# Kernel tuning notes

Hardware: AMD Instinct MI355X
Metric: run time of the kernel (lower is better)

The kernel has to match this reference:

```python
import jax, jax.numpy as jnp
import numpy as np

B, S, F, D, H, L, FF, M, NH, D2, O = 4, 1024, 20, 512, 8, 4, 2048, 32, 3, 256, 1
HD = D // H


def ln(x, g, b, eps=1e-5):
    m = jnp.mean(x, -1, keepdims=True)
    v = jnp.mean((x - m) ** 2, -1, keepdims=True)
    return (x - m) / jnp.sqrt(v + eps) * g + b


def posenc(seq_len, d_model):
    pos = jnp.arange(seq_len, dtype=jnp.float32)[:, None]
    div = jnp.exp(jnp.arange(0, d_model, 2, dtype=jnp.float32) * (-np.log(10000.0) / d_model))
    pe = jnp.zeros((seq_len, d_model), jnp.float32)
    pe = pe.at[:, 0::2].set(jnp.sin(pos * div)).at[:, 1::2].set(jnp.cos(pos * div))
    return pe


def setup_inputs():
    key = jax.random.key(0)
    ks = iter(jax.random.split(key, 64))
    g = lambda shape, s=0.02: jax.random.normal(next(ks), shape, jnp.float32) * s
    z = lambda shape: jnp.zeros(shape, jnp.float32)
    o = lambda shape: jnp.ones(shape, jnp.float32)
    return {
        'x': jax.random.normal(next(ks), (B, S, F), jnp.float32),
        'in_W': g((F, D)), 'in_b': z((D,)), 'in_ln_g': o((D,)), 'in_ln_b': z((D,)),
        'ln1_g': o((L, D)), 'ln1_b': z((L, D)),
        'Wq': g((L, D, D)), 'bq': z((L, D)), 'Wk': g((L, D, D)), 'bk': z((L, D)),
        'Wv': g((L, D, D)), 'bv': z((L, D)), 'Wo': g((L, D, D)), 'bo': z((L, D)),
        'rel': g((L, 2 * M + 1, HD)),
        'ln2_g': o((L, D)), 'ln2_b': z((L, D)),
        'W1': g((L, D, FF)), 'b1': z((L, FF)), 'W2': g((L, FF, D)), 'b2': z((L, D)),
        'gWq': g((D, D)), 'gbq': z((D,)), 'gWk': g((D, D)), 'gbk': z((D,)),
        'gWv': g((D, D)), 'gbv': z((D,)), 'gWo': g((D, D)), 'gbo': z((D,)),
        'hW1': g((NH, D, D2)), 'hb1': z((NH, D2)), 'hln_g': o((NH, D2)), 'hln_b': z((NH, D2)),
        'hW2': g((NH, D2, O)), 'hb2': z((NH, O)),
    }


def _heads(xx, Wq, bq, Wk, bk, Wv, bv):
    # project and split into heads -> [B,H,S,HD]
    q = (xx @ Wq + bq).reshape(B, S, H, HD).transpose(0, 2, 1, 3)
    k = (xx @ Wk + bk).reshape(B, S, H, HD).transpose(0, 2, 1, 3)
    v = (xx @ Wv + bv).reshape(B, S, H, HD).transpose(0, 2, 1, 3)
    return q, k, v


def _block(x, l1g, l1b, Wq, bq, Wk, bk, Wv, bv, Wo, bo, rel, l2g, l2b, W1, b1, W2, b2):
    xn = ln(x, l1g, l1b)
    q, k, v = _heads(xn, Wq, bq, Wk, bk, Wv, bv)
    scores = jnp.einsum('bhqd,bhkd->bhqk', q, k) / jnp.sqrt(jnp.float32(HD))
    pos = jnp.arange(S)
    rel_idx = jnp.clip(pos[None, :] - pos[:, None], -M, M) + M  # [S,S]
    rel_enc = rel[rel_idx]  # [S,S,HD]
    # relative-position bias (NOT scaled by sqrt(HD), matching the torch code)
    scores = scores + jnp.einsum('bhqd,qkd->bhqk', q, rel_enc)
    w = jax.nn.softmax(scores, axis=-1)
    out = jnp.einsum('bhqk,bhkd->bhqd', w, v).transpose(0, 2, 1, 3).reshape(B, S, D)
    x = x + out @ Wo + bo
    xn = ln(x, l2g, l2b)
    ff = jax.nn.gelu(xn @ W1 + b1, approximate=False) @ W2 + b2
    return x + ff


def _forward(x, in_W, in_b, in_ln_g, in_ln_b, ln1_g, ln1_b, Wq, bq, Wk, bk, Wv, bv, Wo, bo, rel,
             ln2_g, ln2_b, W1, b1, W2, b2, gWq, gbq, gWk, gbk, gWv, gbv, gWo, gbo,
             hW1, hb1, hln_g, hln_b, hW2, hb2):
    h = ln(x @ in_W + in_b, in_ln_g, in_ln_b)
    h = h + posenc(S, D)[None]
    for l in range(L):
        h = _block(h, ln1_g[l], ln1_b[l], Wq[l], bq[l], Wk[l], bk[l], Wv[l], bv[l],
                   Wo[l], bo[l], rel[l], ln2_g[l], ln2_b[l], W1[l], b1[l], W2[l], b2[l])
    # global multi-head self-attention (standard scaled dot-product)
    q, k, v = _heads(h, gWq, gbq, gWk, gbk, gWv, gbv)
    w = jax.nn.softmax(jnp.einsum('bhqd,bhkd->bhqk', q, k) / jnp.sqrt(jnp.float32(HD)), axis=-1)
    go = jnp.einsum('bhqk,bhkd->bhqd', w, v).transpose(0, 2, 1, 3).reshape(B, S, D) @ gWo + gbo
    ctx = go[:, -1, :]  # last-timestep context [B,D]
    y = jnp.einsum('bd,hde->bhe', ctx, hW1) + hb1  # [B,NH,D2]
    y = jax.nn.relu(ln(y, hln_g, hln_b))
    return jnp.einsum('bhe,heo->bho', y, hW2) + hb2  # [B,NH,O]


def reference(x, in_W, in_b, in_ln_g, in_ln_b, ln1_g, ln1_b, Wq, bq, Wk, bk, Wv, bv, Wo, bo, rel,
              ln2_g, ln2_b, W1, b1, W2, b2, gWq, gbq, gWk, gbk, gWv, gbv, gWo, gbo,
              hW1, hb1, hln_g, hln_b, hW2, hb2):
    return _forward(x, in_W, in_b, in_ln_g, in_ln_b, ln1_g, ln1_b, Wq, bq, Wk, bk, Wv, bv, Wo, bo,
                    rel, ln2_g, ln2_b, W1, b1, W2, b2, gWq, gbq, gWk, gbk, gWv, gbv, gWo, gbo,
                    hW1, hb1, hln_g, hln_b, hW2, hb2)
```

## Files before the change

kernel.cpp:

```cpp
#include <hip/hip_runtime.h>
#include <math.h>

#define DEV __device__ __forceinline__

constexpr int BSD = 4 * 1024 * 512;

typedef __attribute__((ext_vector_type(8))) short bf16x8;
typedef __attribute__((ext_vector_type(4))) float f32x4;

typedef __attribute__((address_space(1))) const void global_cvoid;
typedef __attribute__((address_space(3))) void lds_void;

DEV ushort f2b(float f) {
  union { float f; uint u; } x{f};
  uint r = x.u + 0x7fff + ((x.u >> 16) & 1);
  return (ushort)(r >> 16);
}
DEV float b2f(ushort u) {
  union { uint u; float f; } x{(uint)u << 16};
  return x.f;
}
DEV int swz128(int b) { return b ^ (((b >> 7) & 7) << 4); }

DEV float wave_sum(float v) {
#pragma unroll
  for (int m = 32; m >= 1; m >>= 1) v += __shfl_xor(v, m, 64);
  return v;
}
DEV float wave_max(float v) {
#pragma unroll
  for (int m = 32; m >= 1; m >>= 1) v = fmaxf(v, __shfl_xor(v, m, 64));
  return v;
}
DEV float block_sum(float v, float* sm) {
  v = wave_sum(v);
  __syncthreads();
  if ((threadIdx.x & 63) == 0) sm[threadIdx.x >> 6] = v;
  __syncthreads();
  return sm[0] + sm[1] + sm[2] + sm[3];
}
DEV float block_max(float v, float* sm) {
  v = wave_max(v);
  __syncthreads();
  if ((threadIdx.x & 63) == 0) sm[threadIdx.x >> 6] = v;
  __syncthreads();
  return fmaxf(fmaxf(sm[0], sm[1]), fmaxf(sm[2], sm[3]));
}

__global__ __launch_bounds__(256) void k_inproj(
    const float* __restrict__ x, const float* __restrict__ W,
    const float* __restrict__ bias, const float* __restrict__ g,
    const float* __restrict__ bt, float* __restrict__ h) {
  int r = blockIdx.x;
  int s = r & 1023;
  int t = threadIdx.x;
  __shared__ float xr[20];
  __shared__ float red[4];
  if (t < 20) xr[t] = x[r * 20 + t];
  __syncthreads();
  float o0 = bias[t], o1 = bias[t + 256];
#pragma unroll
  for (int f = 0; f < 20; f++) {
    float xv = xr[f];
    o0 += xv * W[f * 512 + t];
    o1 += xv * W[f * 512 + t + 256];
  }
  float mean = block_sum(o0 + o1, red) * (1.f / 512.f);
  float d0 = o0 - mean, d1 = o1 - mean;
  float var = block_sum(d0 * d0 + d1 * d1, red) * (1.f / 512.f);
  float rs = rsqrtf(var + 1e-5f);
  float n0 = d0 * rs * g[t] + bt[t];
  float n1 = d1 * rs * g[t + 256] + bt[t + 256];
  const float c1 = -9.210340371976184f / 512.f;
  {
    int c = t;
    float div = expf((float)(c & ~1) * c1);
    float arg = (float)s * div;
    n0 += (c & 1) ? cosf(arg) : sinf(arg);
  }
  {
    int c = t + 256;
    float div = expf((float)(c & ~1) * c1);
    float arg = (float)s * div;
    n1 += (c & 1) ? cosf(arg) : sinf(arg);
  }
  float* hr = h + (size_t)r * 512;
  hr[t] = n0;
  hr[t + 256] = n1;
}

__global__ __launch_bounds__(256) void k_lnw(
    const float* __restrict__ x, const float* __restrict__ g,
    const float* __restrict__ bt, ushort* __restrict__ y) {
  int lane = threadIdx.x & 63;
  int r = blockIdx.x * 4 + (threadIdx.x >> 6);
  const float4* xr = (const float4*)(x + (size_t)r * 512);
  float4 a = xr[lane];
  float4 c = xr[lane + 64];
  float s = a.x + a.y + a.z + a.w + c.x + c.y + c.z + c.w;
  float mean = wave_sum(s) * (1.f / 512.f);
  float d0 = a.x - mean, d1 = a.y - mean, d2 = a.z - mean, d3 = a.w - mean;
  float e0 = c.x - mean, e1 = c.y - mean, e2 = c.z - mean, e3 = c.w - mean;
  float vs = d0 * d0 + d1 * d1 + d2 * d2 + d3 * d3 +
             e0 * e0 + e1 * e1 + e2 * e2 + e3 * e3;
  float var = wave_sum(vs) * (1.f / 512.f);
  float rs = rsqrtf(var + 1e-5f);
  const float4* g4 = (const float4*)g;
  const float4* b4 = (const float4*)bt;
  float4 g0 = g4[lane], g1 = g4[lane + 64];
  float4 b0 = b4[lane], b1 = b4[lane + 64];
  ushort4 o0 = {f2b(d0 * rs * g0.x + b0.x), f2b(d1 * rs * g0.y + b0.y),
                f2b(d2 * rs * g0.z + b0.z), f2b(d3 * rs * g0.w + b0.w)};
  ushort4 o1 = {f2b(e0 * rs * g1.x + b1.x), f2b(e1 * rs * g1.y + b1.y),
                f2b(e2 * rs * g1.z + b1.z), f2b(e3 * rs * g1.w + b1.w)};
  ushort4* yr = (ushort4*)(y + (size_t)r * 512);
  yr[lane] = o0;
  yr[lane + 64] = o1;
}

struct PJobs {
  const float* s[19];
  ushort* d[19];
};
__global__ __launch_bounds__(256) void k_wprep(PJobs j, int K, int N) {
  const float* src = j.s[blockIdx.z];
  ushort* dst = j.d[blockIdx.z];
  __shared__ float ld[32][33];
  int n0 = blockIdx.x * 32, k0 = blockIdx.y * 32;
  int c = threadIdx.x & 31, r0 = threadIdx.x >> 5;
#pragma unroll
  for (int i = 0; i < 4; i++)
    ld[r0 + i * 8][c] = src[(size_t)(k0 + r0 + i * 8) * N + n0 + c];
  __syncthreads();
#pragma unroll
  for (int i = 0; i < 4; i++)
    dst[(size_t)(n0 + r0 + i * 8) * K + k0 + c] = f2b(ld[c][r0 + i * 8]);
}

__global__ __launch_bounds__(256) void k_relprep(const float* __restrict__ rel,
                                                 ushort* __restrict__ relb) {
  int i = blockIdx.x * 256 + threadIdx.x;
  int l = blockIdx.y;
  int r = i >> 6, d = i & 63;
  float v = (r < 65) ? rel[((size_t)l * 65 + r) * 64 + d] * 8.f : 0.f;
  relb[(size_t)l * 80 * 64 + i] = f2b(v);
}

template <int BM, int BN, int MODE, int FUSEB>
__global__ __launch_bounds__(256) void k_mg(
    const ushort* __restrict__ A, const ushort* __restrict__ Bt,
    const float* __restrict__ bias0, const float* __restrict__ bias1,
    const float* __restrict__ bias2, void* __restrict__ Cv,
    ushort* __restrict__ C2, int K, int ldc, int gx) {
  __shared__ __align__(16) ushort As[2][BM * 64];
  __shared__ __align__(16) ushort Bs[2][BN * 64];
  int nwg = gridDim.x;
  int id = blockIdx.x;
  int logical = (id & 7) * (nwg >> 3) + (id >> 3);
  int bx = logical % gx, by = logical / gx;
  int row0 = by * BM, col0 = bx * BN;
  int t = threadIdx.x, lane = t & 63, w = t >> 6;
  int rl15 = lane & 15, l16 = lane >> 4;
  constexpr int WR = (BM == 128 && BN == 128) ? 2 : BM / 32;
  constexpr int WC = 4 / WR;
  constexpr int MI = BM / (WR * 16);
  constexpr int NI = BN / (WC * 16);
  int wr = w % WR, wc = w / WR;
  int wrow = wr * MI * 16;
  int wcol = wc * NI * 16;
  f32x4 acc[MI][NI] = {};

  auto stage = [&](int buf, int kb) {
#pragma unroll
    for (int i = 0; i < BM / 32; i++) {
      int blk = w * (BM / 32) + i;
      int lb = blk * 1024 + lane * 16;
      int lg = swz128(lb);
      int r = lg >> 7, cb = (lg & 127) >> 1;
      __builtin_amdgcn_global_load_lds(
          (global_cvoid*)(A + (size_t)(row0 + r) * K + kb + cb),
          (lds_void*)((char*)As[buf] + blk * 1024), 16, 0, 0);
    }
#pragma unroll
    for (int i = 0; i < BN / 32; i++) {
      int blk = w * (BN / 32) + i;
      int lb = blk * 1024 + lane * 16;
      int lg = swz128(lb);
      int r = lg >> 7, cb = (lg & 127) >> 1;
      __builtin_amdgcn_global_load_lds(
          (global_cvoid*)(Bt + (size_t)(col0 + r) * K + kb + cb),
          (lds_void*)((char*)Bs[buf] + blk * 1024), 16, 0, 0);
    }
  };

  stage(0, 0);
  __syncthreads();
  int nkt = K >> 6;
  for (int kt = 0; kt < nkt; kt++) {
    int cur = kt & 1;
    if (kt + 1 < nkt) stage(cur ^ 1, (kt + 1) << 6);
#pragma unroll
    for (int ks = 0; ks < 2; ks++) {
      bf16x8 af[MI], bfr[NI];
#pragma unroll
      for (int mi = 0; mi < MI; mi++) {
        int row = wrow + mi * 16 + rl15;
        af[mi] =
            *(const bf16x8*)((char*)As[cur] + swz128(row * 128 + ks * 64 + l16 * 16));
      }
#pragma unroll
      for (int ni = 0; ni < NI; ni++) {
        int row = wcol + ni * 16 + rl15;
        bfr[ni] =
            *(const bf16x8*)((char*)Bs[cur] + swz128(row * 128 + ks * 64 + l16 * 16));
      }
#pragma unroll
      for (int mi = 0; mi < MI; mi++)
#pragma unroll
        for (int ni = 0; ni < NI; ni++)
          acc[mi][ni] = __builtin_amdgcn_mfma_f32_16x16x32_bf16(af[mi], bfr[ni],
                                                                acc[mi][ni], 0, 0, 0);
    }
    __syncthreads();
  }
#pragma unroll
  for (int mi = 0; mi < MI; mi++) {
#pragma unroll
    for (int ni = 0; ni < NI; ni++) {
      int col = col0 + wcol + ni * 16 + rl15;
      float bv;
      if (FUSEB) {
        const float* bp = bias0;
        int c = col;
        if (c >= 1024) { bp = bias2; c -= 1024; }
        else if (c >= 512) { bp = bias1; c -= 512; }
        bv = bp[c];
      } else {
        bv = bias0[col];
      }
#pragma unroll
      for (int r = 0; r < 4; r++) {
        int row = row0 + wrow + mi * 16 + l16 * 4 + r;
        float val = acc[mi][ni][r] + bv;
        if (FUSEB && col < 512) val *= 0.125f;
        if (MODE == 0) {
          ushort bval = f2b(val);
          ((ushort*)Cv)[(size_t)row * ldc + col] = bval;
          if (FUSEB && col >= 1024) {
            int dg = col - 1024;
            int bh = (row >> 10) * 8 + (dg >> 6);
            C2[((size_t)bh * 64 + (dg & 63)) * 1024 + (row & 1023)] = bval;
          }
        } else if (MODE == 1) {
          float* Cp = (float*)Cv + (size_t)row * ldc + col;
          *Cp = *Cp + val;
        } else if (MODE == 2) {
          val = 0.5f * val * (1.f + erff(val * 0.70710678118654752f));
          ((ushort*)Cv)[(size_t)row * ldc + col] = f2b(val);
        } else {
          float* Cp = (float*)Cv + (size_t)row * ldc + col;
          float nv = *Cp + val;
          *Cp = nv;
          C2[(size_t)row * ldc + col] = f2b(nv);
        }
      }
    }
  }
}

__global__ __launch_bounds__(256) void k_attn3(
    const ushort* __restrict__ qkv, const ushort* __restrict__ vT,
    const ushort* __restrict__ relb, ushort* __restrict__ ao) {
  __shared__ __align__(16) ushort Ks[2][64 * 64];
  __shared__ __align__(16) ushort Vts[2][64 * 64];
  __shared__ ushort qrlb[4][16][66];
  __shared__ __align__(16) ushort Pl[4][16 * 72];
  int t = threadIdx.x, lane = t & 63, w = t >> 6;
  int bid = blockIdx.x;
  int p = bid & 31;
  int h = p & 7, b = p >> 3;
  int q0 = (bid >> 5) * 64;
  int qw = q0 + w * 16;
  int rl15 = lane & 15, l16 = lane >> 4;
  size_t baseq = ((size_t)b * 1024) * 1536 + h * 64;
  size_t basek = baseq + 512;
  const ushort* vTb = vT + ((size_t)(b * 8 + h)) * 64 * 1024;

  bf16x8 aq[2];
#pragma unroll
  for (int ks = 0; ks < 2; ks++)
    aq[ks] = *(const bf16x8*)(qkv + baseq + (size_t)(qw + rl15) * 1536 + ks * 32 + l16 * 8);

#pragma unroll
  for (int nb = 0; nb < 5; nb++) {
    f32x4 rc = {};
#pragma unroll
    for (int ks = 0; ks < 2; ks++) {
      bf16x8 rb =
          *(const bf16x8*)(relb + (size_t)(nb * 16 + rl15) * 64 + ks * 32 + l16 * 8);
      rc = __builtin_amdgcn_mfma_f32_16x16x32_bf16(aq[ks], rb, rc, 0, 0, 0);
    }
    int col = nb * 16 + rl15;
    if (col < 65) {
#pragma unroll
      for (int r = 0; r < 4; r++) qrlb[w][l16 * 4 + r][col] = f2b(rc[r]);
    }
  }

  auto stage = [&](int buf, int kb) {
#pragma unroll
    for (int i = 0; i < 2; i++) {
      int blk = w * 2 + i;
      int lb = blk * 1024 + lane * 16;
      int lg = swz128(lb);
      int r = lg >> 7, cb = (lg & 127) >> 1;
      __builtin_amdgcn_global_load_lds(
          (global_cvoid*)(qkv + basek + (size_t)(kb + r) * 1536 + cb),
          (lds_void*)((char*)Ks[buf] + blk * 1024), 16, 0, 0);
      __builtin_amdgcn_global_load_lds(
          (global_cvoid*)(vTb + (size_t)r * 1024 + kb + cb),
          (lds_void*)((char*)Vts[buf] + blk * 1024), 16, 0, 0);
    }
  };

  float m_own = -1e30f, l_own = 0.f;
  f32x4 oacc[4] = {};

  stage(0, 0);
  __syncthreads();

  for (int kt = 0; kt < 16; kt++) {
    int kb = kt << 6;
    int cur = kt & 1;
    if (kt < 15) stage(cur ^ 1, kb + 64);

    f32x4 sacc[4] = {};
#pragma unroll
    for (int ks = 0; ks < 2; ks++) {
#pragma unroll
      for (int nb = 0; nb < 4; nb++) {
        bf16x8 kf = *(const bf16x8*)((char*)Ks[cur] +
                                     swz128((nb * 16 + rl15) * 128 + ks * 64 + l16 * 16));
        sacc[nb] = __builtin_amdgcn_mfma_f32_16x16x32_bf16(kf, aq[ks], sacc[nb], 0, 0, 0);
      }
    }

    float sv[4][4];
    bool hiU = (kb >= qw + 47);
    bool loU = (kb + 95 <= qw);
    if (hiU || loU) {
      float crow = b2f(qrlb[w][rl15][hiU ? 64 : 0]);
#pragma unroll
      for (int nb = 0; nb < 4; nb++)
#pragma unroll
        for (int r = 0; r < 4; r++) sv[nb][r] = sacc[nb][r] + crow;
    } else {
      int qg = qw + rl15;
#pragma unroll
      for (int nb = 0; nb < 4; nb++)
#pragma unroll
        for (int r = 0; r < 4; r++) {
          int delta = kb + nb * 16 + l16 * 4 + r - qg;
          delta = delta < -32 ? -32 : (delta > 32 ? 32 : delta);
          sv[nb][r] = sacc[nb][r] + b2f(qrlb[w][rl15][delta + 32]);
        }
    }

    float rowm = sv[0][0];
#pragma unroll
    for (int nb = 0; nb < 4; nb++)
#pragma unroll
      for (int r = 0; r < 4; r++) rowm = fmaxf(rowm, sv[nb][r]);
    rowm = fmaxf(rowm, __shfl_xor(rowm, 16, 64));
    rowm = fmaxf(rowm, __shfl_xor(rowm, 32, 64));

    if (__any(rowm > m_own + 8.f)) {
      float mn = fmaxf(m_own, rowm);
      float sc = __expf(m_own - mn);
      m_own = mn;
      l_own *= sc;
      float s0 = __shfl(sc, l16 * 4 + 0, 64);
      float s1 = __shfl(sc, l16 * 4 + 1, 64);
      float s2 = __shfl(sc, l16 * 4 + 2, 64);
      float s3 = __shfl(sc, l16 * 4 + 3, 64);
#pragma unroll
      for (int nb = 0; nb < 4; nb++) {
        oacc[nb][0] *= s0;
        oacc[nb][1] *= s1;
        oacc[nb][2] *= s2;
        oacc[nb][3] *= s3;
      }
    }

    float pv[4][4];
    float ls = 0.f;
#pragma unroll
    for (int nb = 0; nb < 4; nb++)
#pragma unroll
      for (int r = 0; r < 4; r++) {
        float e = __expf(sv[nb][r] - m_own);
        pv[nb][r] = e;
        ls += e;
      }
    ls += __shfl_xor(ls, 16, 64);
    ls += __shfl_xor(ls, 32, 64);
    l_own += ls;

#pragma unroll
    for (int nb = 0; nb < 4; nb++) {
      uint w0 = (uint)f2b(pv[nb][0]) | ((uint)f2b(pv[nb][1]) << 16);
      uint w1 = (uint)f2b(pv[nb][2]) | ((uint)f2b(pv[nb][3]) << 16);
      uint* dst = (uint*)&Pl[w][rl15 * 72 + nb * 16 + l16 * 4];
      dst[0] = w0;
      dst[1] = w1;
    }
#pragma unroll
    for (int ks = 0; ks < 2; ks++) {
      bf16x8 pa = *(const bf16x8*)&Pl[w][rl15 * 72 + ks * 32 + l16 * 8];
#pragma unroll
      for (int nb = 0; nb < 4; nb++) {
        bf16x8 bv8 = *(const bf16x8*)((char*)Vts[cur] +
                                      swz128((nb * 16 + rl15) * 128 + ks * 64 + l16 * 16));
        oacc[nb] = __builtin_amdgcn_mfma_f32_16x16x32_bf16(pa, bv8, oacc[nb], 0, 0, 0);
      }
    }
    __syncthreads();
  }

  float linv[4];
#pragma unroll
  for (int r = 0; r < 4; r++) linv[r] = 1.f / __shfl(l_own, l16 * 4 + r, 64);
  size_t baseo = ((size_t)b * 1024) * 512 + h * 64;
#pragma unroll
  for (int nb = 0; nb < 4; nb++) {
    int d = nb * 16 + rl15;
#pragma unroll
    for (int r = 0; r < 4; r++) {
      int row = q0 + w * 16 + l16 * 4 + r;
      ao[baseo + (size_t)row * 512 + d] = f2b(oacc[nb][r] * linv[r]);
    }
  }
}

__global__ __launch_bounds__(256) void k_gattn(
    const ushort* __restrict__ qkv, float* __restrict__ ctxa) {
  int t = threadIdx.x;
  int h = blockIdx.x & 7, b = blockIdx.x >> 3;
  __shared__ float Qs[64];
  __shared__ float sc[1024];
  __shared__ float red[4];
  __shared__ float op[4][64];
  if (t < 64) Qs[t] = b2f(qkv[(size_t)(b * 1024 + 1023) * 1536 + h * 64 + t]);
  __syncthreads();
  float lm = -1e30f;
  float sv[4];
#pragma unroll
  for (int jj = 0; jj < 4; jj++) {
    int j = t + (jj << 8);
    float s = 0.f;
#pragma unroll
    for (int d = 0; d < 64; d++)
      s += Qs[d] * b2f(qkv[(size_t)(b * 1024 + j) * 1536 + 512 + h * 64 + d]);
    sv[jj] = s;
    lm = fmaxf(lm, s);
  }
  float bm = block_max(lm, red);
  float ls = 0.f;
#pragma unroll
  for (int jj = 0; jj < 4; jj++) {
    float e = __expf(sv[jj] - bm);
    sc[t + (jj << 8)] = e;
    ls += e;
  }
  float bs = block_sum(ls, red);
  int d = t & 63, qd = t >> 6;
  float acc = 0.f;
  for (int j = qd << 8; j < (qd << 8) + 256; j++)
    acc += sc[j] * b2f(qkv[(size_t)(b * 1024 + j) * 1536 + 1024 + h * 64 + d]);
  op[qd][d] = acc;
  __syncthreads();
  if (t < 64) {
    float r = (op[0][t] + op[1][t] + op[2][t] + op[3][t]) / bs;
    ctxa[b * 512 + h * 64 + t] = r;
  }
}

__global__ __launch_bounds__(256) void k_rowgemm(
    const float* __restrict__ xrow, const float* __restrict__ W,
    const float* __restrict__ bias, float* __restrict__ y) {
  int b = blockIdx.x;
  int t = threadIdx.x;
  __shared__ float xs[512];
  xs[t] = xrow[b * 512 + t];
  xs[t + 256] = xrow[b * 512 + t + 256];
  __syncthreads();
  float a0 = bias[t], a1 = bias[t + 256];
  for (int kk = 0; kk < 512; kk++) {
    float xv = xs[kk];
    a0 += xv * W[(size_t)kk * 512 + t];
    a1 += xv * W[(size_t)kk * 512 + t + 256];
  }
  y[b * 512 + t] = a0;
  y[b * 512 + t + 256] = a1;
}

__global__ __launch_bounds__(256) void k_head(
    const float* __restrict__ ctx, const float* __restrict__ hW1,
    const float* __restrict__ hb1, const float* __restrict__ hg,
    const float* __restrict__ hbt, const float* __restrict__ hW2,
    const float* __restrict__ hb2, float* __restrict__ out) {
  int b = blockIdx.x / 3, nh = blockIdx.x % 3;
  int t = threadIdx.x;
  __shared__ float cs[512];
  __shared__ float red[4];
  cs[t] = ctx[b * 512 + t];
  cs[t + 256] = ctx[b * 512 + t + 256];
  __syncthreads();
  float y = hb1[nh * 256 + t];
  for (int d = 0; d < 512; d++) y += cs[d] * hW1[((size_t)nh * 512 + d) * 256 + t];
  float mean = block_sum(y, red) * (1.f / 256.f);
  float dv = y - mean;
  float var = block_sum(dv * dv, red) * (1.f / 256.f);
  float rs = rsqrtf(var + 1e-5f);
  float yn = dv * rs * hg[nh * 256 + t] + hbt[nh * 256 + t];
  yn = fmaxf(yn, 0.f);
  float s = block_sum(yn * hW2[nh * 256 + t], red);
  if (t == 0) out[b * 3 + nh] = s + hb2[nh];
}

extern "C" void kernel_launch(void* const* d_in, const int* in_sizes, int n_in,
                              void* d_out, int out_size, void* d_ws, size_t ws_size,
                              hipStream_t stream) {
  const float* x = (const float*)d_in[0];
  const float* in_W = (const float*)d_in[1];
  const float* in_b = (const float*)d_in[2];
  const float* in_lng = (const float*)d_in[3];
  const float* in_lnb = (const float*)d_in[4];
  const float* ln1_g = (const float*)d_in[5];
  const float* ln1_b = (const float*)d_in[6];
  const float* Wq = (const float*)d_in[7];
  const float* bq = (const float*)d_in[8];
  const float* Wk = (const float*)d_in[9];
  const float* bk = (const float*)d_in[10];
  const float* Wv = (const float*)d_in[11];
  const float* bv = (const float*)d_in[12];
  const float* Wo = (const float*)d_in[13];
  const float* bo = (const float*)d_in[14];
  const float* rel = (const float*)d_in[15];
  const float* ln2_g = (const float*)d_in[16];
  const float* ln2_b = (const float*)d_in[17];
  const float* W1 = (const float*)d_in[18];
  const float* b1 = (const float*)d_in[19];
  const float* W2 = (const float*)d_in[20];
  const float* b2 = (const float*)d_in[21];
  const float* gWq = (const float*)d_in[22];
  const float* gbq = (const float*)d_in[23];
  const float* gWk = (const float*)d_in[24];
  const float* gbk = (const float*)d_in[25];
  const float* gWv = (const float*)d_in[26];
  const float* gbv = (const float*)d_in[27];
  const float* gWo = (const float*)d_in[28];
  const float* gbo = (const float*)d_in[29];
  const float* hW1 = (const float*)d_in[30];
  const float* hb1 = (const float*)d_in[31];
  const float* hlng = (const float*)d_in[32];
  const float* hlnb = (const float*)d_in[33];
  const float* hW2 = (const float*)d_in[34];
  const float* hb2 = (const float*)d_in[35];
  float* out = (float*)d_out;

  uint8_t* wsb = (uint8_t*)d_ws;
  const size_t MB = 1024 * 1024;
  float* h = (float*)(wsb + 0);
  ushort* xn = (ushort*)(wsb + 8 * MB);
  ushort* qkvb = (ushort*)(wsb + 12 * MB);
  ushort* aob = (ushort*)(wsb + 24 * MB);
  ushort* ffb = (ushort*)(wsb + 28 * MB);
  ushort* vTb = ffb;
  ushort* wqkv = (ushort*)(wsb + 44 * MB);
  ushort* wto = (ushort*)(wsb + 50 * MB);
  ushort* wt1 = (ushort*)(wsb + 52 * MB);
  ushort* wt2 = (ushort*)(wsb + 60 * MB);
  ushort* gwqkv = (ushort*)(wsb + 68 * MB);
  ushort* relb = (ushort*)(wsb + 70 * MB);
  float* attnlast = (float*)(wsb + 71 * MB);
  float* ctx = attnlast + 4096;

  const size_t W55 = 512 * 512;

  {
    PJobs j{};
    for (int l = 0; l < 4; l++) {
      j.s[l * 4 + 0] = Wq + (size_t)l * W55;
      j.d[l * 4 + 0] = wqkv + (size_t)l * 1536 * 512;
      j.s[l * 4 + 1] = Wk + (size_t)l * W55;
      j.d[l * 4 + 1] = wqkv + (size_t)l * 1536 * 512 + 512 * 512;
      j.s[l * 4 + 2] = Wv + (size_t)l * W55;
      j.d[l * 4 + 2] = wqkv + (size_t)l * 1536 * 512 + 1024 * 512;
      j.s[l * 4 + 3] = Wo + (size_t)l * W55;
      j.d[l * 4 + 3] = wto + (size_t)l * W55;
    }
    j.s[16] = gWq; j.d[16] = gwqkv;
    j.s[17] = gWk; j.d[17] = gwqkv + 512 * 512;
    j.s[18] = gWv; j.d[18] = gwqkv + 1024 * 512;
    k_wprep<<<dim3(16, 16, 19), 256, 0, stream>>>(j, 512, 512);
  }
  {
    PJobs j{};
    for (int l = 0; l < 4; l++) {
      j.s[l] = W1 + (size_t)l * 512 * 2048;
      j.d[l] = wt1 + (size_t)l * 2048 * 512;
    }
    k_wprep<<<dim3(64, 16, 4), 256, 0, stream>>>(j, 512, 2048);
  }
  {
    PJobs j{};
    for (int l = 0; l < 4; l++) {
      j.s[l] = W2 + (size_t)l * 2048 * 512;
      j.d[l] = wt2 + (size_t)l * 512 * 2048;
    }
    k_wprep<<<dim3(16, 64, 4), 256, 0, stream>>>(j, 2048, 512);
  }
  k_relprep<<<dim3(20, 4), 256, 0, stream>>>(rel, relb);
  k_inproj<<<4096, 256, 0, stream>>>(x, in_W, in_b, in_lng, in_lnb, h);

  for (int l = 0; l < 4; l++) {
    size_t vo = (size_t)l * 512;
    k_lnw<<<1024, 256, 0, stream>>>(h, ln1_g + vo, ln1_b + vo, xn);
    k_mg<128, 64, 0, 1><<<768, 256, 0, stream>>>(xn, wqkv + (size_t)l * 1536 * 512,
                                                 bq + vo, bk + vo, bv + vo, qkvb,
                                                 vTb, 512, 1536, 24);
    k_attn3<<<512, 256, 0, stream>>>(qkvb, vTb, relb + (size_t)l * 80 * 64, aob);
    k_mg<64, 64, 1, 0><<<512, 256, 0, stream>>>(aob, wto + (size_t)l * W55, bo + vo,
                                                nullptr, nullptr, h, nullptr, 512, 512, 8);
    k_lnw<<<1024, 256, 0, stream>>>(h, ln2_g + vo, ln2_b + vo, xn);
    k_mg<128, 128, 2, 0><<<512, 256, 0, stream>>>(xn, wt1 + (size_t)l * 2048 * 512,
                                                  b1 + (size_t)l * 2048, nullptr, nullptr,
                                                  ffb, nullptr, 512, 2048, 16);
    if (l < 3)
      k_mg<64, 64, 1, 0><<<512, 256, 0, stream>>>(ffb, wt2 + (size_t)l * 512 * 2048,
                                                  b2 + vo, nullptr, nullptr, h, nullptr,
                                                  2048, 512, 8);
    else
      k_mg<64, 64, 3, 0><<<512, 256, 0, stream>>>(ffb, wt2 + (size_t)l * 512 * 2048,
                                                  b2 + vo, nullptr, nullptr, h, xn,
                                                  2048, 512, 8);
  }

  k_mg<128, 64, 0, 1><<<768, 256, 0, stream>>>(xn, gwqkv, gbq, gbk, gbv, qkvb,
                                               vTb, 512, 1536, 24);
  k_gattn<<<32, 256, 0, stream>>>(qkvb, attnlast);
  k_rowgemm<<<4, 256, 0, stream>>>(attnlast, gWo, gbo, ctx);
  k_head<<<12, 256, 0, stream>>>(ctx, hW1, hb1, hlng, hlnb, hW2, hb2, out);
}
```

Baseline: 554.9 us.

## Triple-buffer LDS staging in GEMM and attention with explicit vmcnt waits

Moves the GEMM and relative-attention kernels from double to triple buffering of LDS tiles. Loads are issued two tiles ahead and each iteration waits with s_waitcnt vmcnt plus a single barrier, replacing the two-barrier double-buffer scheme. The attention kernel also issues its first K/V loads before the rel-position prologue so that prologue overlaps the loads. The FFN1 GEMM switches to a 128x64 tile with twice the workgroups. In exchange, LDS use per block grows, which may lower occupancy, and correctness now depends on the vmcnt constants matching the number of loads per stage.

```diff
diff --git a/kernel.cpp b/kernel.cpp
--- a/kernel.cpp
+++ b/kernel.cpp
@@ -21,6 +21,16 @@
   return x.f;
 }
 DEV int swz128(int b) { return b ^ (((b >> 7) & 7) << 4); }
+
+template <int N>
+DEV void vmwait() {
+  asm volatile("s_waitcnt vmcnt(%0)" ::"i"(N) : "memory");
+}
+DEV void sbar() {
+  __builtin_amdgcn_sched_barrier(0);
+  __builtin_amdgcn_s_barrier();
+  __builtin_amdgcn_sched_barrier(0);
+}
 
 DEV float wave_sum(float v) {
 #pragma unroll
@@ -152,8 +162,9 @@
     const float* __restrict__ bias0, const float* __restrict__ bias1,
     const float* __restrict__ bias2, void* __restrict__ Cv,
     ushort* __restrict__ C2, int K, int ldc, int gx) {
-  __shared__ __align__(16) ushort As[2][BM * 64];
-  __shared__ __align__(16) ushort Bs[2][BN * 64];
+  __shared__ __align__(16) ushort As[3][BM * 64];
+  __shared__ __align__(16) ushort Bs[3][BN * 64];
+  constexpr int L = BM / 32 + BN / 32;
   int nwg = gridDim.x;
   int id = blockIdx.x;
   int logical = (id & 7) * (nwg >> 3) + (id >> 3);
@@ -193,12 +204,7 @@
     }
   };
 
-  stage(0, 0);
-  __syncthreads();
-  int nkt = K >> 6;
-  for (int kt = 0; kt < nkt; kt++) {
-    int cur = kt & 1;
-    if (kt + 1 < nkt) stage(cur ^ 1, (kt + 1) << 6);
+  auto compute = [&](int buf) {
 #pragma unroll
     for (int ks = 0; ks < 2; ks++) {
       bf16x8 af[MI], bfr[NI];
@@ -206,13 +212,13 @@
       for (int mi = 0; mi < MI; mi++) {
         int row = wrow + mi * 16 + rl15;
         af[mi] =
-            *(const bf16x8*)((char*)As[cur] + swz128(row * 128 + ks * 64 + l16 * 16));
+            *(const bf16x8*)((char*)As[buf] + swz128(row * 128 + ks * 64 + l16 * 16));
       }
 #pragma unroll
       for (int ni = 0; ni < NI; ni++) {
         int row = wcol + ni * 16 + rl15;
         bfr[ni] =
-            *(const bf16x8*)((char*)Bs[cur] + swz128(row * 128 + ks * 64 + l16 * 16));
+            *(const bf16x8*)((char*)Bs[buf] + swz128(row * 128 + ks * 64 + l16 * 16));
       }
 #pragma unroll
       for (int mi = 0; mi < MI; mi++)
@@ -221,8 +227,24 @@
           acc[mi][ni] = __builtin_amdgcn_mfma_f32_16x16x32_bf16(af[mi], bfr[ni],
                                                                 acc[mi][ni], 0, 0, 0);
     }
-    __syncthreads();
-  }
+  };
+
+  int nkt = K >> 6;
+  stage(0, 0);
+  stage(1, 64);
+  vmwait<L>();
+  sbar();
+  for (int kt = 0; kt + 2 < nkt; kt++) {
+    stage((kt + 2) % 3, (kt + 2) << 6);
+    compute(kt % 3);
+    vmwait<L>();
+    sbar();
+  }
+  compute((nkt - 2) % 3);
+  vmwait<0>();
+  sbar();
+  compute((nkt - 1) % 3);
+
 #pragma unroll
   for (int mi = 0; mi < MI; mi++) {
 #pragma unroll
@@ -271,8 +293,8 @@
 __global__ __launch_bounds__(256) void k_attn3(
     const ushort* __restrict__ qkv, const ushort* __restrict__ vT,
     const ushort* __restrict__ relb, ushort* __restrict__ ao) {
-  __shared__ __align__(16) ushort Ks[2][64 * 64];
-  __shared__ __align__(16) ushort Vts[2][64 * 64];
+  __shared__ __align__(16) ushort Ks[3][64 * 64];
+  __shared__ __align__(16) ushort Vts[3][64 * 64];
   __shared__ ushort qrlb[4][16][66];
   __shared__ __align__(16) ushort Pl[4][16 * 72];
   int t = threadIdx.x, lane = t & 63, w = t >> 6;
@@ -291,22 +313,6 @@
   for (int ks = 0; ks < 2; ks++)
     aq[ks] = *(const bf16x8*)(qkv + baseq + (size_t)(qw + rl15) * 1536 + ks * 32 + l16 * 8);
 
-#pragma unroll
-  for (int nb = 0; nb < 5; nb++) {
-    f32x4 rc = {};
-#pragma unroll
-    for (int ks = 0; ks < 2; ks++) {
-      bf16x8 rb =
-          *(const bf16x8*)(relb + (size_t)(nb * 16 + rl15) * 64 + ks * 32 + l16 * 8);
-      rc = __builtin_amdgcn_mfma_f32_16x16x32_bf16(aq[ks], rb, rc, 0, 0, 0);
-    }
-    int col = nb * 16 + rl15;
-    if (col < 65) {
-#pragma unroll
-      for (int r = 0; r < 4; r++) qrlb[w][l16 * 4 + r][col] = f2b(rc[r]);
-    }
-  }
-
   auto stage = [&](int buf, int kb) {
 #pragma unroll
     for (int i = 0; i < 2; i++) {
@@ -323,23 +329,36 @@
     }
   };
 
+  stage(0, 0);
+  stage(1, 64);
+
+#pragma unroll
+  for (int nb = 0; nb < 5; nb++) {
+    f32x4 rc = {};
+#pragma unroll
+    for (int ks = 0; ks < 2; ks++) {
+      bf16x8 rb =
+          *(const bf16x8*)(relb + (size_t)(nb * 16 + rl15) * 64 + ks * 32 + l16 * 8);
+      rc = __builtin_amdgcn_mfma_f32_16x16x32_bf16(aq[ks], rb, rc, 0, 0, 0);
+    }
+    int col = nb * 16 + rl15;
+    if (col < 65) {
+#pragma unroll
+      for (int r = 0; r < 4; r++) qrlb[w][l16 * 4 + r][col] = f2b(rc[r]);
+    }
+  }
+
   float m_own = -1e30f, l_own = 0.f;
   f32x4 oacc[4] = {};
 
-  stage(0, 0);
-  __syncthreads();
-
-  for (int kt = 0; kt < 16; kt++) {
+  auto compute = [&](int kt, int buf) {
     int kb = kt << 6;
-    int cur = kt & 1;
-    if (kt < 15) stage(cur ^ 1, kb + 64);
-
     f32x4 sacc[4] = {};
 #pragma unroll
     for (int ks = 0; ks < 2; ks++) {
 #pragma unroll
       for (int nb = 0; nb < 4; nb++) {
-        bf16x8 kf = *(const bf16x8*)((char*)Ks[cur] +
+        bf16x8 kf = *(const bf16x8*)((char*)Ks[buf] +
                                      swz128((nb * 16 + rl15) * 128 + ks * 64 + l16 * 16));
         sacc[nb] = __builtin_amdgcn_mfma_f32_16x16x32_bf16(kf, aq[ks], sacc[nb], 0, 0, 0);
       }
@@ -419,13 +438,25 @@
       bf16x8 pa = *(const bf16x8*)&Pl[w][rl15 * 72 + ks * 32 + l16 * 8];
 #pragma unroll
       for (int nb = 0; nb < 4; nb++) {
-        bf16x8 bv8 = *(const bf16x8*)((char*)Vts[cur] +
+        bf16x8 bv8 = *(const bf16x8*)((char*)Vts[buf] +
                                       swz128((nb * 16 + rl15) * 128 + ks * 64 + l16 * 16));
         oacc[nb] = __builtin_amdgcn_mfma_f32_16x16x32_bf16(pa, bv8, oacc[nb], 0, 0, 0);
       }
     }
-    __syncthreads();
-  }
+  };
+
+  vmwait<4>();
+  sbar();
+  for (int kt = 0; kt + 2 < 16; kt++) {
+    stage((kt + 2) % 3, (kt + 2) << 6);
+    compute(kt, kt % 3);
+    vmwait<4>();
+    sbar();
+  }
+  compute(14, 14 % 3);
+  vmwait<0>();
+  sbar();
+  compute(15, 15 % 3);
 
   float linv[4];
 #pragma unroll
@@ -634,9 +665,9 @@
     k_mg<64, 64, 1, 0><<<512, 256, 0, stream>>>(aob, wto + (size_t)l * W55, bo + vo,
                                                 nullptr, nullptr, h, nullptr, 512, 512, 8);
     k_lnw<<<1024, 256, 0, stream>>>(h, ln2_g + vo, ln2_b + vo, xn);
-    k_mg<128, 128, 2, 0><<<512, 256, 0, stream>>>(xn, wt1 + (size_t)l * 2048 * 512,
+    k_mg<128, 64, 2, 0><<<1024, 256, 0, stream>>>(xn, wt1 + (size_t)l * 2048 * 512,
                                                   b1 + (size_t)l * 2048, nullptr, nullptr,
-                                                  ffb, nullptr, 512, 2048, 16);
+                                                  ffb, nullptr, 512, 2048, 32);
     if (l < 3)
       k_mg<64, 64, 1, 0><<<512, 256, 0, stream>>>(ffb, wt2 + (size_t)l * 512 * 2048,
                                                   b2 + vo, nullptr, nullptr, h, nullptr,
```

Result: slower. 609.9 us (median of 3 runs) (+9.9%).
